# Optimization experiments

Hardware: AMD Instinct MI355X
Metric: run time of the kernel (lower is better)

Reference implementation:

```python
import jax, jax.numpy as jnp
import numpy as np

B, D, E, K = 16384, 1024, 8, 2  # tokens, embed_size, experts, top-k
W_IMPORTANCE = 0.01


def setup_inputs() -> dict:
    key = jax.random.key(0)
    ks = jax.random.split(key, 8)
    s = 1.0 / np.sqrt(D)
    return {
        "x": jax.random.normal(ks[0], (B, D), dtype=jnp.float32),   # fused vision features
        "q": jax.random.normal(ks[1], (B, D), dtype=jnp.float32),   # text features
        # cross-attention (seq_len=1) collapses to V then output projection
        "Wv": jax.random.normal(ks[2], (D, D), dtype=jnp.float32) * s,
        "bv": jnp.zeros((D,), dtype=jnp.float32),
        "Wo": jax.random.normal(ks[3], (D, D), dtype=jnp.float32) * s,
        "bo": jnp.zeros((D,), dtype=jnp.float32),
        # gate linear
        "Wg": jax.random.normal(ks[4], (D, E), dtype=jnp.float32) * s,
        "bg": jnp.zeros((E,), dtype=jnp.float32),
        # experts: Linear -> SiLU -> Linear
        "W1": jax.random.normal(ks[5], (E, D, D), dtype=jnp.float32) * s,
        "b1": jnp.zeros((E, D), dtype=jnp.float32),
        "W2": jax.random.normal(ks[6], (E, D, D), dtype=jnp.float32) * s,
        "b2": jnp.zeros((E, D), dtype=jnp.float32),
    }


def reference(x, q, Wv, bv, Wo, bo, Wg, bg, W1, b1, W2, b2):
    # CrossAttention with q_len = kv_len = 1: softmax over a single key is 1,
    # so attention output = out_proj(V(q)).
    att = (q @ Wv + bv) @ Wo + bo                      # (B, D)
    gate_logits = att @ Wg + bg                        # (B, E)
    gate_prob = jax.nn.softmax(gate_logits, axis=-1)   # eval mode: no noise
    top_w, top_i = jax.lax.top_k(gate_prob, K)         # (B, K)
    top_w = jax.nn.softmax(top_w, axis=-1)             # renormalize over top-k

    y = jnp.zeros_like(x)
    for e in range(E):  # small fixed expert count
        w_e = jnp.sum(jnp.where(top_i == e, top_w, 0.0), axis=-1)  # (B,)
        h = jax.nn.silu(x @ W1[e] + b1[e]) @ W2[e] + b2[e]         # (B, D)
        y = y + w_e[:, None] * h

    importance = gate_prob.sum(axis=0)  # (E,)
    importance_loss = W_IMPORTANCE * (jnp.std(importance, ddof=1) / jnp.mean(importance)) ** 2
    return y, gate_prob, importance_loss
```

## Files before the change

kernel.cpp:

```cpp
#include <hip/hip_runtime.h>
#include <hip/hip_bf16.h>

#define Btok 16384
#define Ddim 1024
#define Eexp 8

typedef __attribute__((ext_vector_type(8))) short short8;
typedef __attribute__((ext_vector_type(4))) float f32x4;

__device__ inline unsigned short f2bf(float f) {
    unsigned int u = __float_as_uint(f);
    unsigned int r = (u + 0x7fffu + ((u >> 16) & 1u)) >> 16;
    return (unsigned short)r;
}

__device__ inline void gload16(const void* g, void* l) {
    __builtin_amdgcn_global_load_lds(
        (const __attribute__((address_space(1))) void*)g,
        (__attribute__((address_space(3))) void*)l, 16, 0, 0);
}

__global__ __launch_bounds__(256) void k_tmp(const float* __restrict__ Wo,
                                             const float* __restrict__ Wg,
                                             float* __restrict__ tmp) {
    int id = blockIdx.x * 256 + threadIdx.x;
    int d = id >> 3, e = id & 7;
    double s = 0.0;
    for (int k = 0; k < Ddim; ++k)
        s += (double)Wo[(long)d * Ddim + k] * (double)Wg[k * Eexp + e];
    tmp[id] = (float)s;
}

__global__ __launch_bounds__(256) void k_wc(const float* __restrict__ Wv,
                                            const float* __restrict__ tmp,
                                            float* __restrict__ WcT) {
    int id = blockIdx.x * 256 + threadIdx.x;
    int d = id >> 3, e = id & 7;
    double s = 0.0;
    for (int k = 0; k < Ddim; ++k)
        s += (double)Wv[(long)d * Ddim + k] * (double)tmp[k * Eexp + e];
    WcT[e * Ddim + d] = (float)s;
}

__global__ __launch_bounds__(512) void k_bc(const float* __restrict__ bv,
                                            const float* __restrict__ bo,
                                            const float* __restrict__ bg,
                                            const float* __restrict__ Wg,
                                            const float* __restrict__ tmp,
                                            float* __restrict__ bcomb) {
    int w = threadIdx.x >> 6, l = threadIdx.x & 63;
    double s = 0.0;
    for (int k = l; k < Ddim; k += 64)
        s += (double)bv[k] * (double)tmp[k * Eexp + w] +
             (double)bo[k] * (double)Wg[k * Eexp + w];
    #pragma unroll
    for (int off = 32; off; off >>= 1) s += __shfl_xor(s, off);
    if (l == 0) bcomb[w] = (float)s + bg[w];
}

__global__ __launch_bounds__(256) void k_convx(const float4* __restrict__ x,
                                               ushort4* __restrict__ xb) {
    int i = blockIdx.x * 256 + threadIdx.x;
    float4 v = x[i];
    ushort4 o;
    o.x = f2bf(v.x); o.y = f2bf(v.y); o.z = f2bf(v.z); o.w = f2bf(v.w);
    xb[i] = o;
}

__global__ __launch_bounds__(256) void k_convw(const float* __restrict__ W1,
                                               const float* __restrict__ W2,
                                               unsigned short* __restrict__ w1bT,
                                               unsigned short* __restrict__ w2bT) {
    __shared__ float tile[32][33];
    int bid = blockIdx.x;
    int arr = bid >> 13;
    int e = (bid >> 10) & 7, bi = (bid >> 5) & 31, bj = bid & 31;
    const float* src = (arr ? W2 : W1) + (long)e * Ddim * Ddim;
    unsigned short* dst = (arr ? w2bT : w1bT) + (long)e * Ddim * Ddim;
    int tr = threadIdx.x >> 5, tc = threadIdx.x & 31;
    #pragma unroll
    for (int i = 0; i < 4; ++i) {
        int dl = tr + i * 8;
        tile[dl][tc] = src[(long)(bi * 32 + dl) * Ddim + bj * 32 + tc];
    }
    __syncthreads();
    #pragma unroll
    for (int i = 0; i < 4; ++i) {
        int nl = tr + i * 8;
        dst[(long)(bj * 32 + nl) * Ddim + bi * 32 + tc] = f2bf(tile[tc][nl]);
    }
}

__global__ __launch_bounds__(256) void k_gate(const float* __restrict__ q,
                                              const float* __restrict__ WcT,
                                              const float* __restrict__ bcomb,
                                              float* __restrict__ gate_prob,
                                              int* __restrict__ choice,
                                              float2* __restrict__ w12,
                                              float* __restrict__ impP) {
    __shared__ float impL[4][8];
    int w = threadIdx.x >> 6, l = threadIdx.x & 63;
    int t = blockIdx.x * 4 + w;
    const float* qr = q + (long)t * Ddim;
    float acc[8] = {0, 0, 0, 0, 0, 0, 0, 0};
    #pragma unroll
    for (int i = 0; i < 4; ++i) {
        float4 qv = *(const float4*)(qr + (i * 64 + l) * 4);
        #pragma unroll
        for (int e = 0; e < 8; ++e) {
            float4 wv = *(const float4*)(WcT + e * Ddim + (i * 64 + l) * 4);
            acc[e] += qv.x * wv.x + qv.y * wv.y + qv.z * wv.z + qv.w * wv.w;
        }
    }
    #pragma unroll
    for (int off = 32; off; off >>= 1)
        #pragma unroll
        for (int e = 0; e < 8; ++e) acc[e] += __shfl_xor(acc[e], off);
    float lg[8], p[8];
    float m = -1e30f;
    #pragma unroll
    for (int e = 0; e < 8; ++e) { lg[e] = acc[e] + bcomb[e]; m = fmaxf(m, lg[e]); }
    float s = 0.f;
    #pragma unroll
    for (int e = 0; e < 8; ++e) { p[e] = expf(lg[e] - m); s += p[e]; }
    float inv = 1.f / s;
    #pragma unroll
    for (int e = 0; e < 8; ++e) p[e] *= inv;
    float p1 = -1.f, p2 = -1.f; int i1 = 0, i2 = 0;
    #pragma unroll
    for (int e = 0; e < 8; ++e) {
        float pe = p[e];
        if (pe > p1) { p2 = p1; i2 = i1; p1 = pe; i1 = e; }
        else if (pe > p2) { p2 = pe; i2 = e; }
    }
    float ee = expf(p2 - p1);
    float wa = 1.f / (1.f + ee);
    float wb = ee / (1.f + ee);
    if (l == 0) {
        #pragma unroll
        for (int e = 0; e < 8; ++e) gate_prob[(long)t * 8 + e] = p[e];
        #pragma unroll
        for (int e = 0; e < 8; ++e) impL[w][e] = p[e];
        choice[t] = i1 | (i2 << 8);
        w12[t] = make_float2(wa, wb);
    }
    __syncthreads();
    if (threadIdx.x < 8)
        impP[blockIdx.x * 8 + threadIdx.x] =
            impL[0][threadIdx.x] + impL[1][threadIdx.x] +
            impL[2][threadIdx.x] + impL[3][threadIdx.x];
}

__global__ __launch_bounds__(256) void k_hist(const int* __restrict__ choice,
                                              int* __restrict__ bcnt) {
    __shared__ int cnt[8];
    if (threadIdx.x < 8) cnt[threadIdx.x] = 0;
    __syncthreads();
    int ch = choice[blockIdx.x * 256 + threadIdx.x];
    atomicAdd(&cnt[ch & 255], 1);
    atomicAdd(&cnt[(ch >> 8) & 255], 1);
    __syncthreads();
    if (threadIdx.x < 8) bcnt[blockIdx.x * 8 + threadIdx.x] = cnt[threadIdx.x];
}

__global__ __launch_bounds__(512) void k_scan(const int* __restrict__ bcnt,
                                              int* __restrict__ bbase,
                                              int* __restrict__ counts) {
    int w = threadIdx.x >> 6, l = threadIdx.x & 63;
    int v = bcnt[l * 8 + w];
    int s = v;
    #pragma unroll
    for (int off = 1; off < 64; off <<= 1) {
        int o = __shfl_up(s, off);
        if (l >= off) s += o;
    }
    bbase[l * 8 + w] = s - v;
    if (l == 63) counts[w] = s;
}

__global__ __launch_bounds__(256) void k_scatter(const int* __restrict__ choice,
                                                 const float2* __restrict__ w12,
                                                 const int* __restrict__ bbase,
                                                 int* __restrict__ tok,
                                                 float* __restrict__ wgt) {
    __shared__ int wsum[4];
    int w = threadIdx.x >> 6, l = threadIdx.x & 63;
    int t = blockIdx.x * 256 + threadIdx.x;
    int ch = choice[t];
    int i1 = ch & 255, i2 = (ch >> 8) & 255;
    float2 ww = w12[t];
    for (int e = 0; e < 8; ++e) {
        bool f1 = (i1 == e), f2 = (i2 == e);
        bool f = f1 || f2;
        unsigned long long m = __ballot(f);
        int wl = __popcll(m & ((1ull << l) - 1ull));
        if (l == 0) wsum[w] = (int)__popcll(m);
        __syncthreads();
        int before = 0;
        #pragma unroll
        for (int j = 0; j < 4; ++j) before += (j < w) ? wsum[j] : 0;
        if (f) {
            int p = bbase[blockIdx.x * 8 + e] + before + wl;
            tok[e * Btok + p] = t;
            wgt[e * Btok + p] = f1 ? ww.x : ww.y;
        }
        __syncthreads();
    }
}

template <int MODE>
__global__ __launch_bounds__(256, 4) void k_gemm(const unsigned short* __restrict__ Abase,
                                                 const unsigned short* __restrict__ WT,
                                                 const float* __restrict__ bias,
                                                 const int* __restrict__ counts,
                                                 const int* __restrict__ tok,
                                                 const float* __restrict__ wgt,
                                                 unsigned short* __restrict__ Hout,
                                                 float* __restrict__ y) {
    __shared__ __align__(16) char lds[32768];
    char* ldsp = (char*)lds;

    int bid = blockIdx.x;
    int e = bid & 7;
    int k = bid >> 3;
    int group = k >> 5;
    int inner = k & 31;
    int rt = (group >> 1) * 8 + (inner & 7);
    int ct = (group & 1) * 4 + (inner >> 3);

    int n_e = counts[e];
    int r0 = rt * 128;
    if (r0 >= n_e) return;
    int off_e = 0;
    #pragma unroll
    for (int j = 0; j < 8; ++j) off_e += (j < e) ? counts[j] : 0;
    int n0 = ct * 128;

    int t = threadIdx.x;
    int w = t >> 6, l = t & 63;
    int wm = w >> 1, wn = w & 1;

    int tr = t >> 3;
    int sc = (t & 7) ^ (tr & 7);
    const char* srcA[4]; const char* srcB[4];
    #pragma unroll
    for (int ri = 0; ri < 4; ++ri) {
        int idx = r0 + ri * 32 + tr; if (idx > n_e - 1) idx = n_e - 1;
        long g = (MODE == 0) ? (long)tok[e * Btok + idx] : (long)(off_e + idx);
        srcA[ri] = (const char*)Abase + g * 2048 + sc * 16;
        srcB[ri] = (const char*)WT + ((long)e << 21) + (long)(n0 + ri * 32 + tr) * 2048 + sc * 16;
    }
    int dstoff = tr * 128 + (t & 7) * 16;

    int rA = (wm * 64 + (l & 15)) * 128;
    int rB = (wn * 64 + (l & 15)) * 128;
    int x0 = ((l >> 4) ^ (l & 7)) << 4;
    int x1 = (((l >> 4) + 4) ^ (l & 7)) << 4;

    f32x4 acc[4][4];
    #pragma unroll
    for (int mi = 0; mi < 4; ++mi)
        #pragma unroll
        for (int ni = 0; ni < 4; ++ni) acc[mi][ni] = {0.f, 0.f, 0.f, 0.f};

    const int NT = Ddim / 64;
    for (int kk = 0; kk < NT; ++kk) {
        #pragma unroll
        for (int ri = 0; ri < 4; ++ri) {
            gload16(srcA[ri], ldsp + ri * 4096 + dstoff);
            gload16(srcB[ri], ldsp + 16384 + ri * 4096 + dstoff);
            srcA[ri] += 128; srcB[ri] += 128;
        }
        __syncthreads();
        #pragma unroll
        for (int ks = 0; ks < 2; ++ks) {
            int xo = ks ? x1 : x0;
            short8 av[4], bv[4];
            #pragma unroll
            for (int mi = 0; mi < 4; ++mi)
                av[mi] = *(const short8*)(ldsp + rA + mi * 2048 + xo);
            #pragma unroll
            for (int ni = 0; ni < 4; ++ni)
                bv[ni] = *(const short8*)(ldsp + 16384 + rB + ni * 2048 + xo);
            #pragma unroll
            for (int mi = 0; mi < 4; ++mi)
                #pragma unroll
                for (int ni = 0; ni < 4; ++ni)
                    acc[mi][ni] = __builtin_amdgcn_mfma_f32_16x16x32_bf16(av[mi], bv[ni], acc[mi][ni], 0, 0, 0);
        }
        __syncthreads();
    }

    float bias4[4];
    #pragma unroll
    for (int ni = 0; ni < 4; ++ni)
        bias4[ni] = bias[e * Ddim + n0 + wn * 64 + ni * 16 + (l & 15)];

    #pragma unroll
    for (int mi = 0; mi < 4; ++mi) {
        #pragma unroll
        for (int j = 0; j < 4; ++j) {
            int rl = wm * 64 + mi * 16 + (l >> 4) * 4 + j;
            int r = r0 + rl;
            bool ok = r < n_e;
            int trow = 0; float wr = 0.f;
            if (MODE == 1) {
                int ri = ok ? r : 0;
                trow = tok[e * Btok + ri];
                wr = wgt[e * Btok + ri];
            }
            #pragma unroll
            for (int ni = 0; ni < 4; ++ni) {
                int col = n0 + wn * 64 + ni * 16 + (l & 15);
                float v = acc[mi][ni][j] + bias4[ni];
                if (MODE == 0) {
                    v = v / (1.f + __expf(-v));
                    if (ok) Hout[(long)(off_e + r) * Ddim + col] = f2bf(v);
                } else {
                    if (ok) atomicAdd(&y[(long)trow * Ddim + col], wr * v);
                }
            }
        }
    }
}

__global__ __launch_bounds__(256) void k_loss(const float* __restrict__ impP,
                                              float* __restrict__ out) {
    __shared__ float red[256];
    __shared__ float impF[8];
    for (int e = 0; e < 8; ++e) {
        float s = 0.f;
        for (int i = threadIdx.x; i < 4096; i += 256) s += impP[i * 8 + e];
        red[threadIdx.x] = s;
        __syncthreads();
        for (int st = 128; st > 0; st >>= 1) {
            if ((int)threadIdx.x < st) red[threadIdx.x] += red[threadIdx.x + st];
            __syncthreads();
        }
        if (threadIdx.x == 0) impF[e] = red[0];
        __syncthreads();
    }
    if (threadIdx.x == 0) {
        double mean = 0.0;
        for (int e = 0; e < 8; ++e) mean += (double)impF[e];
        mean /= 8.0;
        double var = 0.0;
        for (int e = 0; e < 8; ++e) {
            double d = (double)impF[e] - mean;
            var += d * d;
        }
        var /= 7.0;
        out[0] = (float)(0.01 * var / (mean * mean));
    }
}

extern "C" void kernel_launch(void* const* d_in, const int* in_sizes, int n_in,
                              void* d_out, int out_size, void* d_ws, size_t ws_size,
                              hipStream_t stream) {
    const float* x  = (const float*)d_in[0];
    const float* q  = (const float*)d_in[1];
    const float* Wv = (const float*)d_in[2];
    const float* bv = (const float*)d_in[3];
    const float* Wo = (const float*)d_in[4];
    const float* bo = (const float*)d_in[5];
    const float* Wg = (const float*)d_in[6];
    const float* bg = (const float*)d_in[7];
    const float* W1 = (const float*)d_in[8];
    const float* b1 = (const float*)d_in[9];
    const float* W2 = (const float*)d_in[10];
    const float* b2 = (const float*)d_in[11];

    float* y = (float*)d_out;
    float* gate_prob = y + (long)Btok * Ddim;
    float* loss = gate_prob + (long)Btok * Eexp;

    char* ws = (char*)d_ws;
    int*   counts = (int*)(ws + 0);
    float* bcomb  = (float*)(ws + 256);
    float* tmp    = (float*)(ws + 512);
    float* WcT    = (float*)(ws + 33280);
    float* impP   = (float*)(ws + 66048);
    int*   choice = (int*)(ws + 197120);
    float2* w12   = (float2*)(ws + 262656);
    int*   tok    = (int*)(ws + 393728);
    float* wgt    = (float*)(ws + 918016);
    int*   bcnt   = (int*)(ws + 1442304);
    int*   bbase  = (int*)(ws + 1444352);
    unsigned short* xb   = (unsigned short*)(ws + 1446912);
    unsigned short* w1bT = (unsigned short*)(ws + 35001344);
    unsigned short* w2bT = (unsigned short*)(ws + 51778560);
    unsigned short* H    = (unsigned short*)(ws + 68555776);

    hipMemsetAsync(y, 0, (size_t)Btok * Ddim * sizeof(float), stream);

    k_tmp<<<32, 256, 0, stream>>>(Wo, Wg, tmp);
    k_wc <<<32, 256, 0, stream>>>(Wv, tmp, WcT);
    k_bc <<<1, 512, 0, stream>>>(bv, bo, bg, Wg, tmp, bcomb);
    k_convx<<<16384, 256, 0, stream>>>((const float4*)x, (ushort4*)xb);
    k_convw<<<16384, 256, 0, stream>>>(W1, W2, w1bT, w2bT);
    k_gate<<<4096, 256, 0, stream>>>(q, WcT, bcomb, gate_prob, choice, w12, impP);
    k_hist<<<64, 256, 0, stream>>>(choice, bcnt);
    k_scan<<<1, 512, 0, stream>>>(bcnt, bbase, counts);
    k_scatter<<<64, 256, 0, stream>>>(choice, w12, bbase, tok, wgt);
    k_gemm<0><<<4096, 256, 0, stream>>>(xb, w1bT, b1, counts, tok, wgt, H, nullptr);
    k_gemm<1><<<4096, 256, 0, stream>>>(H, w2bT, b2, counts, tok, wgt, nullptr, y);
    k_loss<<<1, 256, 0, stream>>>(impP, loss);
}
```

Measured before the change: 456.2 us.

## Enlarge expert GEMM tiles to 256x256 with double-buffered LDS pipeline

Rewrites the grouped expert GEMM to use 512-thread blocks computing 256x256 output tiles, with a two-stage double-buffered LDS pipeline that issues global-to-LDS loads for the next K tile while MFMAs run on the current one. Uses explicit vmcnt waits, raw barriers, and s_setprio around MFMA bursts. This targets the exposed load latency and extra LDS traffic of the previous single-buffered 128x128 tiling. The cost is 128KB of LDS per block and more accumulator registers, which lowers occupancy, and coarser tiles waste more work on partial expert row tiles.

```diff
diff --git a/kernel.cpp b/kernel.cpp
--- a/kernel.cpp
+++ b/kernel.cpp
@@ -19,6 +19,11 @@
         (const __attribute__((address_space(1))) void*)g,
         (__attribute__((address_space(3))) void*)l, 16, 0, 0);
 }
+
+#define MEMF() asm volatile("" ::: "memory")
+#define BARRIER() do { MEMF(); __builtin_amdgcn_s_barrier(); MEMF(); } while (0)
+#define VMW(n) do { asm volatile("s_waitcnt vmcnt(" #n ")" ::: "memory"); \
+                    __builtin_amdgcn_sched_barrier(0); } while (0)
 
 __global__ __launch_bounds__(256) void k_tmp(const float* __restrict__ Wo,
                                              const float* __restrict__ Wg,
@@ -209,7 +214,7 @@
 }
 
 template <int MODE>
-__global__ __launch_bounds__(256, 4) void k_gemm(const unsigned short* __restrict__ Abase,
+__global__ __launch_bounds__(512, 2) void k_gemm(const unsigned short* __restrict__ Abase,
                                                  const unsigned short* __restrict__ WT,
                                                  const float* __restrict__ bias,
                                                  const int* __restrict__ counts,
@@ -217,90 +222,125 @@
                                                  const float* __restrict__ wgt,
                                                  unsigned short* __restrict__ Hout,
                                                  float* __restrict__ y) {
-    __shared__ __align__(16) char lds[32768];
+    __shared__ __align__(16) char lds[131072];
     char* ldsp = (char*)lds;
 
     int bid = blockIdx.x;
     int e = bid & 7;
     int k = bid >> 3;
-    int group = k >> 5;
-    int inner = k & 31;
-    int rt = (group >> 1) * 8 + (inner & 7);
-    int ct = (group & 1) * 4 + (inner >> 3);
+    int rt = k >> 2, ct = k & 3;
 
     int n_e = counts[e];
-    int r0 = rt * 128;
+    int r0 = rt * 256;
     if (r0 >= n_e) return;
     int off_e = 0;
     #pragma unroll
     for (int j = 0; j < 8; ++j) off_e += (j < e) ? counts[j] : 0;
-    int n0 = ct * 128;
+    int n0 = ct * 256;
 
     int t = threadIdx.x;
     int w = t >> 6, l = t & 63;
-    int wm = w >> 1, wn = w & 1;
-
-    int tr = t >> 3;
-    int sc = (t & 7) ^ (tr & 7);
-    const char* srcA[4]; const char* srcB[4];
-    #pragma unroll
-    for (int ri = 0; ri < 4; ++ri) {
-        int idx = r0 + ri * 32 + tr; if (idx > n_e - 1) idx = n_e - 1;
-        long g = (MODE == 0) ? (long)tok[e * Btok + idx] : (long)(off_e + idx);
-        srcA[ri] = (const char*)Abase + g * 2048 + sc * 16;
-        srcB[ri] = (const char*)WT + ((long)e << 21) + (long)(n0 + ri * 32 + tr) * 2048 + sc * 16;
-    }
-    int dstoff = tr * 128 + (t & 7) * 16;
-
-    int rA = (wm * 64 + (l & 15)) * 128;
-    int rB = (wn * 64 + (l & 15)) * 128;
-    int x0 = ((l >> 4) ^ (l & 7)) << 4;
-    int x1 = (((l >> 4) + 4) ^ (l & 7)) << 4;
-
-    f32x4 acc[4][4];
-    #pragma unroll
-    for (int mi = 0; mi < 4; ++mi)
-        #pragma unroll
-        for (int ni = 0; ni < 4; ++ni) acc[mi][ni] = {0.f, 0.f, 0.f, 0.f};
+    int wm = w >> 2, wn = w & 3;
+
+    const char* sA[2]; const char* sB[2];
+    {
+        int cpos = t & 3;
+        #pragma unroll
+        for (int j = 0; j < 2; ++j) {
+            int r = (t >> 2) + j * 128;
+            int cg = cpos ^ ((r >> 1) & 3);
+            int idx = r0 + r; if (idx > n_e - 1) idx = n_e - 1;
+            long g = (MODE == 0) ? (long)tok[e * Btok + idx] : (long)(off_e + idx);
+            sA[j] = (const char*)Abase + g * 2048 + cg * 16;
+            sB[j] = (const char*)WT + ((long)e << 21) + (long)(n0 + r) * 2048 + cg * 16;
+        }
+    }
+    int dstoff = w * 1024;
+
+    int laneoff = (l & 15) * 64 + (((l >> 4) ^ (((l & 15) >> 1) & 3)) << 4);
+
+    f32x4 acc[8][4];
+    #pragma unroll
+    for (int fi = 0; fi < 8; ++fi)
+        #pragma unroll
+        for (int nf = 0; nf < 4; ++nf) acc[fi][nf] = {0.f, 0.f, 0.f, 0.f};
+
+    short8 av[8], bv[2];
+
+    auto stageA = [&](int kh, int nb, int kt) {
+        char* d = ldsp + nb * 32768 + kh * 16384 + dstoff;
+        gload16(sA[0] + kt * 128 + kh * 64, d);
+        gload16(sA[1] + kt * 128 + kh * 64, d + 8192);
+    };
+    auto stageB = [&](int kh, int nb, int kt) {
+        char* d = ldsp + 65536 + nb * 32768 + kh * 16384 + dstoff;
+        gload16(sB[0] + kt * 128 + kh * 64, d);
+        gload16(sB[1] + kt * 128 + kh * 64, d + 8192);
+    };
+    auto readAV = [&](int buf, int kh) {
+        const char* p = ldsp + buf * 32768 + kh * 16384 + wm * 8192 + laneoff;
+        #pragma unroll
+        for (int fi = 0; fi < 8; ++fi) av[fi] = *(const short8*)(p + fi * 1024);
+    };
+    auto readBV = [&](int buf, int kh, int nh) {
+        const char* p = ldsp + 65536 + buf * 32768 + kh * 16384 + wn * 4096 + nh * 2048 + laneoff;
+        bv[0] = *(const short8*)(p);
+        bv[1] = *(const short8*)(p + 1024);
+    };
+
+#define MFMA_NH(nh) do { \
+        __builtin_amdgcn_s_setprio(1); \
+        _Pragma("unroll") \
+        for (int fi_ = 0; fi_ < 8; ++fi_) { \
+            acc[fi_][(nh)*2+0] = __builtin_amdgcn_mfma_f32_16x16x32_bf16(av[fi_], bv[0], acc[fi_][(nh)*2+0], 0, 0, 0); \
+            acc[fi_][(nh)*2+1] = __builtin_amdgcn_mfma_f32_16x16x32_bf16(av[fi_], bv[1], acc[fi_][(nh)*2+1], 0, 0, 0); \
+        } \
+        __builtin_amdgcn_s_setprio(0); } while (0)
 
     const int NT = Ddim / 64;
-    for (int kk = 0; kk < NT; ++kk) {
-        #pragma unroll
-        for (int ri = 0; ri < 4; ++ri) {
-            gload16(srcA[ri], ldsp + ri * 4096 + dstoff);
-            gload16(srcB[ri], ldsp + 16384 + ri * 4096 + dstoff);
-            srcA[ri] += 128; srcB[ri] += 128;
-        }
-        __syncthreads();
-        #pragma unroll
-        for (int ks = 0; ks < 2; ++ks) {
-            int xo = ks ? x1 : x0;
-            short8 av[4], bv[4];
-            #pragma unroll
-            for (int mi = 0; mi < 4; ++mi)
-                av[mi] = *(const short8*)(ldsp + rA + mi * 2048 + xo);
-            #pragma unroll
-            for (int ni = 0; ni < 4; ++ni)
-                bv[ni] = *(const short8*)(ldsp + 16384 + rB + ni * 2048 + xo);
-            #pragma unroll
-            for (int mi = 0; mi < 4; ++mi)
-                #pragma unroll
-                for (int ni = 0; ni < 4; ++ni)
-                    acc[mi][ni] = __builtin_amdgcn_mfma_f32_16x16x32_bf16(av[mi], bv[ni], acc[mi][ni], 0, 0, 0);
-        }
-        __syncthreads();
-    }
+    stageA(0, 0, 0); stageB(0, 0, 0); stageA(1, 0, 0); stageB(1, 0, 0);
+
+    for (int kt = 0; kt < NT - 1; ++kt) {
+        int buf = kt & 1, nb = buf ^ 1;
+        VMW(4); BARRIER();
+        readAV(buf, 0); readBV(buf, 0, 0);
+        stageA(0, nb, kt + 1);
+        MFMA_NH(0);
+        readBV(buf, 0, 1);
+        stageB(0, nb, kt + 1);
+        MFMA_NH(1);
+        VMW(4); BARRIER();
+        readAV(buf, 1); readBV(buf, 1, 0);
+        stageA(1, nb, kt + 1);
+        MFMA_NH(0);
+        readBV(buf, 1, 1);
+        stageB(1, nb, kt + 1);
+        MFMA_NH(1);
+    }
+    {
+        VMW(4); BARRIER();
+        readAV(1, 0); readBV(1, 0, 0);
+        MFMA_NH(0);
+        readBV(1, 0, 1);
+        MFMA_NH(1);
+        VMW(0); BARRIER();
+        readAV(1, 1); readBV(1, 1, 0);
+        MFMA_NH(0);
+        readBV(1, 1, 1);
+        MFMA_NH(1);
+    }
+#undef MFMA_NH
 
     float bias4[4];
     #pragma unroll
-    for (int ni = 0; ni < 4; ++ni)
-        bias4[ni] = bias[e * Ddim + n0 + wn * 64 + ni * 16 + (l & 15)];
-
-    #pragma unroll
-    for (int mi = 0; mi < 4; ++mi) {
+    for (int nf = 0; nf < 4; ++nf)
+        bias4[nf] = bias[e * Ddim + n0 + wn * 64 + nf * 16 + (l & 15)];
+
+    #pragma unroll
+    for (int fi = 0; fi < 8; ++fi) {
         #pragma unroll
         for (int j = 0; j < 4; ++j) {
-            int rl = wm * 64 + mi * 16 + (l >> 4) * 4 + j;
+            int rl = wm * 128 + fi * 16 + (l >> 4) * 4 + j;
             int r = r0 + rl;
             bool ok = r < n_e;
             int trow = 0; float wr = 0.f;
@@ -310,9 +350,9 @@
                 wr = wgt[e * Btok + ri];
             }
             #pragma unroll
-            for (int ni = 0; ni < 4; ++ni) {
-                int col = n0 + wn * 64 + ni * 16 + (l & 15);
-                float v = acc[mi][ni][j] + bias4[ni];
+            for (int nf = 0; nf < 4; ++nf) {
+                int col = n0 + wn * 64 + nf * 16 + (l & 15);
+                float v = acc[fi][nf][j] + bias4[nf];
                 if (MODE == 0) {
                     v = v / (1.f + __expf(-v));
                     if (ok) Hout[(long)(off_e + r) * Ddim + col] = f2bf(v);
@@ -402,7 +442,7 @@
     k_hist<<<64, 256, 0, stream>>>(choice, bcnt);
     k_scan<<<1, 512, 0, stream>>>(bcnt, bbase, counts);
     k_scatter<<<64, 256, 0, stream>>>(choice, w12, bbase, tok, wgt);
-    k_gemm<0><<<4096, 256, 0, stream>>>(xb, w1bT, b1, counts, tok, wgt, H, nullptr);
-    k_gemm<1><<<4096, 256, 0, stream>>>(H, w2bT, b2, counts, tok, wgt, nullptr, y);
+    k_gemm<0><<<1024, 512, 0, stream>>>(xb, w1bT, b1, counts, tok, wgt, H, nullptr);
+    k_gemm<1><<<1024, 512, 0, stream>>>(H, w2bT, b2, counts, tok, wgt, nullptr, y);
     k_loss<<<1, 256, 0, stream>>>(impP, loss);
 }
```

Measured after the change: 518.8 us. 1.14x slower.

## Prefetch GEMM tiles through registers with software pipelining instead of direct-to-LDS loads

Applied to the files above, without the earlier changes.

Replaces the global_load_lds path with register-staged loads. The tile two steps ahead is fetched into registers while the current LDS tile is consumed, then written to LDS between barriers, so global latency overlaps the MFMA work. It also raises wave priority around the MFMA block and switches the block-to-tile mapping from a grouped swizzle to plain row-major. The costs are 8 int4 staging registers per thread, which may reduce occupancy, and possibly worse L2 reuse from dropping the grouped ordering.

```diff
diff --git a/kernel.cpp b/kernel.cpp
--- a/kernel.cpp
+++ b/kernel.cpp
@@ -14,11 +14,9 @@
     return (unsigned short)r;
 }
 
-__device__ inline void gload16(const void* g, void* l) {
-    __builtin_amdgcn_global_load_lds(
-        (const __attribute__((address_space(1))) void*)g,
-        (__attribute__((address_space(3))) void*)l, 16, 0, 0);
-}
+#define MEMF() asm volatile("" ::: "memory")
+#define BARRIER() do { MEMF(); __builtin_amdgcn_s_barrier(); MEMF(); } while (0)
+#define LGKM0() asm volatile("s_waitcnt lgkmcnt(0)" ::: "memory")
 
 __global__ __launch_bounds__(256) void k_tmp(const float* __restrict__ Wo,
                                              const float* __restrict__ Wg,
@@ -223,10 +221,7 @@
     int bid = blockIdx.x;
     int e = bid & 7;
     int k = bid >> 3;
-    int group = k >> 5;
-    int inner = k & 31;
-    int rt = (group >> 1) * 8 + (inner & 7);
-    int ct = (group & 1) * 4 + (inner >> 3);
+    int rt = k >> 3, ct = k & 7;
 
     int n_e = counts[e];
     int r0 = rt * 128;
@@ -241,16 +236,19 @@
     int wm = w >> 1, wn = w & 1;
 
     int tr = t >> 3;
-    int sc = (t & 7) ^ (tr & 7);
-    const char* srcA[4]; const char* srcB[4];
+    int ch = t & 7;
+    const char* sA[4]; const char* sB[4];
     #pragma unroll
     for (int ri = 0; ri < 4; ++ri) {
         int idx = r0 + ri * 32 + tr; if (idx > n_e - 1) idx = n_e - 1;
         long g = (MODE == 0) ? (long)tok[e * Btok + idx] : (long)(off_e + idx);
-        srcA[ri] = (const char*)Abase + g * 2048 + sc * 16;
-        srcB[ri] = (const char*)WT + ((long)e << 21) + (long)(n0 + ri * 32 + tr) * 2048 + sc * 16;
-    }
-    int dstoff = tr * 128 + (t & 7) * 16;
+        sA[ri] = (const char*)Abase + g * 2048 + ch * 16;
+        sB[ri] = (const char*)WT + ((long)e << 21) + (long)(n0 + ri * 32 + tr) * 2048 + ch * 16;
+    }
+    int pc = ch ^ (tr & 7);
+    int dst[4];
+    #pragma unroll
+    for (int ri = 0; ri < 4; ++ri) dst[ri] = (ri * 32 + tr) * 128 + pc * 16;
 
     int rA = (wm * 64 + (l & 15)) * 128;
     int rB = (wn * 64 + (l & 15)) * 128;
@@ -263,15 +261,29 @@
         #pragma unroll
         for (int ni = 0; ni < 4; ++ni) acc[mi][ni] = {0.f, 0.f, 0.f, 0.f};
 
+    int4 stg[8];
+
+#define LOADT(kt) do { \
+        _Pragma("unroll") \
+        for (int ri_ = 0; ri_ < 4; ++ri_) { \
+            stg[ri_]     = *(const int4*)(sA[ri_] + (kt) * 128); \
+            stg[ri_ + 4] = *(const int4*)(sB[ri_] + (kt) * 128); \
+        } } while (0)
+#define DSWRITE() do { \
+        _Pragma("unroll") \
+        for (int ri_ = 0; ri_ < 4; ++ri_) { \
+            *(int4*)(ldsp + dst[ri_])         = stg[ri_]; \
+            *(int4*)(ldsp + 16384 + dst[ri_]) = stg[ri_ + 4]; \
+        } } while (0)
+
     const int NT = Ddim / 64;
-    for (int kk = 0; kk < NT; ++kk) {
-        #pragma unroll
-        for (int ri = 0; ri < 4; ++ri) {
-            gload16(srcA[ri], ldsp + ri * 4096 + dstoff);
-            gload16(srcB[ri], ldsp + 16384 + ri * 4096 + dstoff);
-            srcA[ri] += 128; srcB[ri] += 128;
-        }
-        __syncthreads();
+    LOADT(0);
+    DSWRITE();
+    LOADT(1);
+    LGKM0();
+    BARRIER();
+
+    for (int kt = 0; kt < NT; ++kt) {
         #pragma unroll
         for (int ks = 0; ks < 2; ++ks) {
             int xo = ks ? x1 : x0;
@@ -282,14 +294,23 @@
             #pragma unroll
             for (int ni = 0; ni < 4; ++ni)
                 bv[ni] = *(const short8*)(ldsp + 16384 + rB + ni * 2048 + xo);
+            __builtin_amdgcn_s_setprio(1);
             #pragma unroll
             for (int mi = 0; mi < 4; ++mi)
                 #pragma unroll
                 for (int ni = 0; ni < 4; ++ni)
                     acc[mi][ni] = __builtin_amdgcn_mfma_f32_16x16x32_bf16(av[mi], bv[ni], acc[mi][ni], 0, 0, 0);
-        }
-        __syncthreads();
-    }
+            __builtin_amdgcn_s_setprio(0);
+        }
+        if (kt == NT - 1) break;
+        BARRIER();
+        DSWRITE();
+        if (kt < NT - 2) LOADT(kt + 2);
+        LGKM0();
+        BARRIER();
+    }
+#undef LOADT
+#undef DSWRITE
 
     float bias4[4];
     #pragma unroll
```

New measurement: 921.2 us. +101.9%, slower.

## Double-buffer expert GEMM K-loop with async LDS loads and simplified tile order

Applied to the files above, without the earlier changes.

Restructures the expert GEMM main loop from a single-buffered 64-wide K step into a two-stage pipeline of 32-wide K steps. The next tile's global-to-LDS loads are issued while the current one is computed, with explicit vmcnt waits and raw barriers, and MFMA issue priority is raised. It also changes the LDS layout and swizzle to match, and replaces the grouped block-to-tile mapping with a plain row-major one. This aims to hide global memory latency, at the cost of more barriers per unit of K work and possibly worse L2 reuse from the simpler tile order.

```diff
diff --git a/kernel.cpp b/kernel.cpp
--- a/kernel.cpp
+++ b/kernel.cpp
@@ -19,6 +19,11 @@
         (const __attribute__((address_space(1))) void*)g,
         (__attribute__((address_space(3))) void*)l, 16, 0, 0);
 }
+
+#define MEMF() asm volatile("" ::: "memory")
+#define BARRIER() do { MEMF(); __builtin_amdgcn_s_barrier(); MEMF(); } while (0)
+#define VMW(n) do { asm volatile("s_waitcnt vmcnt(" #n ")" ::: "memory"); \
+                    __builtin_amdgcn_sched_barrier(0); } while (0)
 
 __global__ __launch_bounds__(256) void k_tmp(const float* __restrict__ Wo,
                                              const float* __restrict__ Wg,
@@ -223,10 +228,7 @@
     int bid = blockIdx.x;
     int e = bid & 7;
     int k = bid >> 3;
-    int group = k >> 5;
-    int inner = k & 31;
-    int rt = (group >> 1) * 8 + (inner & 7);
-    int ct = (group & 1) * 4 + (inner >> 3);
+    int rt = k >> 3, ct = k & 7;
 
     int n_e = counts[e];
     int r0 = rt * 128;
@@ -239,23 +241,25 @@
     int t = threadIdx.x;
     int w = t >> 6, l = t & 63;
     int wm = w >> 1, wn = w & 1;
-
-    int tr = t >> 3;
-    int sc = (t & 7) ^ (tr & 7);
-    const char* srcA[4]; const char* srcB[4];
-    #pragma unroll
-    for (int ri = 0; ri < 4; ++ri) {
-        int idx = r0 + ri * 32 + tr; if (idx > n_e - 1) idx = n_e - 1;
-        long g = (MODE == 0) ? (long)tok[e * Btok + idx] : (long)(off_e + idx);
-        srcA[ri] = (const char*)Abase + g * 2048 + sc * 16;
-        srcB[ri] = (const char*)WT + ((long)e << 21) + (long)(n0 + ri * 32 + tr) * 2048 + sc * 16;
-    }
-    int dstoff = tr * 128 + (t & 7) * 16;
-
-    int rA = (wm * 64 + (l & 15)) * 128;
-    int rB = (wn * 64 + (l & 15)) * 128;
-    int x0 = ((l >> 4) ^ (l & 7)) << 4;
-    int x1 = (((l >> 4) + 4) ^ (l & 7)) << 4;
+    int t16 = t * 16;
+
+    const char* sA[2]; const char* sB[2];
+    {
+        int q = (t & 7) ^ ((t >> 3) & 7);
+        int h = q >> 2, c = q & 3;
+        #pragma unroll
+        for (int r = 0; r < 2; ++r) {
+            int rowl = (t >> 3) + 32 * r + 64 * h;
+            int idx = r0 + rowl; if (idx > n_e - 1) idx = n_e - 1;
+            long g = (MODE == 0) ? (long)tok[e * Btok + idx] : (long)(off_e + idx);
+            sA[r] = (const char*)Abase + g * 2048 + c * 16;
+            sB[r] = (const char*)WT + ((long)e << 21) + (long)(n0 + rowl) * 2048 + c * 16;
+        }
+    }
+
+    int rowb = (l & 15) * 128;
+    int cpA = (((wm << 2) | (l >> 4)) ^ (l & 7)) << 4;
+    int cpB = (((wn << 2) | (l >> 4)) ^ (l & 7)) << 4;
 
     f32x4 acc[4][4];
     #pragma unroll
@@ -263,33 +267,41 @@
         #pragma unroll
         for (int ni = 0; ni < 4; ++ni) acc[mi][ni] = {0.f, 0.f, 0.f, 0.f};
 
-    const int NT = Ddim / 64;
-    for (int kk = 0; kk < NT; ++kk) {
-        #pragma unroll
-        for (int ri = 0; ri < 4; ++ri) {
-            gload16(srcA[ri], ldsp + ri * 4096 + dstoff);
-            gload16(srcB[ri], ldsp + 16384 + ri * 4096 + dstoff);
-            srcA[ri] += 128; srcB[ri] += 128;
-        }
-        __syncthreads();
-        #pragma unroll
-        for (int ks = 0; ks < 2; ++ks) {
-            int xo = ks ? x1 : x0;
-            short8 av[4], bv[4];
-            #pragma unroll
-            for (int mi = 0; mi < 4; ++mi)
-                av[mi] = *(const short8*)(ldsp + rA + mi * 2048 + xo);
+    auto stage = [&](int b) {
+        gload16(sA[0], ldsp + b * 8192 + t16);
+        gload16(sA[1], ldsp + b * 8192 + 4096 + t16);
+        gload16(sB[0], ldsp + 16384 + b * 8192 + t16);
+        gload16(sB[1], ldsp + 16384 + b * 8192 + 4096 + t16);
+        sA[0] += 64; sA[1] += 64; sB[0] += 64; sB[1] += 64;
+    };
+    auto compute = [&](int b) {
+        const char* pA = ldsp + b * 8192 + rowb;
+        const char* pB = ldsp + 16384 + b * 8192 + rowb;
+        short8 av[4], bv[4];
+        #pragma unroll
+        for (int mi = 0; mi < 4; ++mi) av[mi] = *(const short8*)(pA + mi * 2048 + cpA);
+        #pragma unroll
+        for (int ni = 0; ni < 4; ++ni) bv[ni] = *(const short8*)(pB + ni * 2048 + cpB);
+        __builtin_amdgcn_s_setprio(1);
+        #pragma unroll
+        for (int mi = 0; mi < 4; ++mi)
             #pragma unroll
             for (int ni = 0; ni < 4; ++ni)
-                bv[ni] = *(const short8*)(ldsp + 16384 + rB + ni * 2048 + xo);
-            #pragma unroll
-            for (int mi = 0; mi < 4; ++mi)
-                #pragma unroll
-                for (int ni = 0; ni < 4; ++ni)
-                    acc[mi][ni] = __builtin_amdgcn_mfma_f32_16x16x32_bf16(av[mi], bv[ni], acc[mi][ni], 0, 0, 0);
-        }
-        __syncthreads();
-    }
+                acc[mi][ni] = __builtin_amdgcn_mfma_f32_16x16x32_bf16(av[mi], bv[ni], acc[mi][ni], 0, 0, 0);
+        __builtin_amdgcn_s_setprio(0);
+    };
+
+    stage(0);
+    stage(1);
+    for (int kk = 0; kk < 31; ++kk) {
+        VMW(4);
+        BARRIER();
+        compute(kk & 1);
+        BARRIER();
+        if (kk < 30) stage(kk & 1);
+    }
+    VMW(0); BARRIER();
+    compute(1);
 
     float bias4[4];
     #pragma unroll
```

New measurement: 456.1 us. Within noise of the previous version (-0.0%).
